# Performance work log

Hardware: AMD Instinct MI355X
Metric: run time of the kernel (lower is better)

## Reference

```python
import jax, jax.numpy as jnp
import numpy as np

N_NODES = 50000
N_EDGES = 800000
IN_FEATS = 128
HIDDEN = 256
N_CLASSES = 64


def setup_inputs() -> dict:
    key = jax.random.key(0)
    ks = jax.random.split(key, 16)
    def w(k, shape, fan_in):
        return jax.random.normal(k, shape, dtype=jnp.float32) * (1.0 / np.sqrt(fan_in))
    inp = {
        "x": jax.random.normal(ks[0], (N_NODES, IN_FEATS), dtype=jnp.float32),
        "edge_src": jax.random.randint(ks[1], (N_EDGES,), 0, N_NODES, dtype=jnp.int32),
        "edge_dst": jax.random.randint(ks[2], (N_EDGES,), 0, N_NODES, dtype=jnp.int32),
        # layer 0: in_feats -> hidden
        "W0s": w(ks[3], (IN_FEATS, HIDDEN), IN_FEATS),
        "W0n": w(ks[4], (IN_FEATS, HIDDEN), IN_FEATS),
        "b0": jnp.zeros((HIDDEN,), dtype=jnp.float32),
        # layer 1: hidden -> hidden
        "W1s": w(ks[5], (HIDDEN, HIDDEN), HIDDEN),
        "W1n": w(ks[6], (HIDDEN, HIDDEN), HIDDEN),
        "b1": jnp.zeros((HIDDEN,), dtype=jnp.float32),
        # layer 2: hidden -> hidden (last conv also outputs hidden per source code)
        "W2s": w(ks[7], (HIDDEN, HIDDEN), HIDDEN),
        "W2n": w(ks[8], (HIDDEN, HIDDEN), HIDDEN),
        "b2": jnp.zeros((HIDDEN,), dtype=jnp.float32),
        # fc1: hidden -> n_classes
        "Wfc": w(ks[9], (HIDDEN, N_CLASSES), HIDDEN),
        "bfc": jnp.zeros((N_CLASSES,), dtype=jnp.float32),
    }
    return inp


def _sage_layer(h, src, dst, Ws, Wn, b):
    # mean-neighbor aggregation: segment-sum messages, divide by in-degree
    msg = h[src]  # [E, D] irregular gather
    agg = jax.ops.segment_sum(msg, dst, num_segments=N_NODES)  # [N, D]
    deg = jax.ops.segment_sum(jnp.ones_like(dst, dtype=h.dtype), dst, num_segments=N_NODES)
    h_neigh = agg / jnp.maximum(deg, 1.0)[:, None]
    # DGL SAGEConv (mean): fc_self(h) + fc_neigh(h_neigh) + bias
    return h @ Ws + h_neigh @ Wn + b


def reference(x, edge_src, edge_dst, W0s, W0n, b0, W1s, W1n, b1, W2s, W2n, b2, Wfc, bfc):
    # forward applies dropout (identity at eval) and NO activation between layers,
    # matching the original module's forward().
    h = _sage_layer(x, edge_src, edge_dst, W0s, W0n, b0)
    h = _sage_layer(h, edge_src, edge_dst, W1s, W1n, b1)
    h = _sage_layer(h, edge_src, edge_dst, W2s, W2n, b2)
    return h @ Wfc + bfc  # [N, n_classes]
```

## Files before the change

kernel.cpp:

```cpp
#include <hip/hip_runtime.h>

#define NN 50000
#define NE 800000
#define F_IN 128
#define HID 256
#define N_CLS 64
#define SCAN_BLOCKS ((NN + 255) / 256)
#define HEPT 2
#define HBF ((NE + 256 * HEPT - 1) / (256 * HEPT))
#define CF_BLOCKS 36
#define CL_BLOCKS 9
#define GA_BLOCKS ((NN + 127) / 128)
#define GG_BLOCKS ((NN + 31) / 32)
#define CROWS 515

typedef _Float16 half8 __attribute__((ext_vector_type(8)));
typedef float f32x4 __attribute__((ext_vector_type(4)));

__device__ __forceinline__ const float* virtC1_row(int r, const float* W0s,
                                                   const float* W0n, const float* b0) {
    if (r < 0) return nullptr;
    if (r < 128) return W0s + (size_t)r * 256;
    if (r < 256) return W0n + (size_t)(r - 128) * 256;
    if (r == 512) return b0;
    return nullptr;
}

__device__ __forceinline__ int shift_src(int r) {
    if (r >= 128 && r < 512) return r - 128;
    if (r == 513) return 512;
    if (r == 514) return 513;
    return -1;
}

__device__ __forceinline__ void compose_first_dev(
    int bx, const float* __restrict__ W0s, const float* __restrict__ W0n,
    const float* __restrict__ b0,
    const float* __restrict__ B1, const float* __restrict__ B2,
    const float* __restrict__ brow, float* __restrict__ C)
{
    __shared__ float As[64][17];
    __shared__ float Bs[16][64];
    const int tid = threadIdx.x;
    const int tx = tid & 15, ty = tid >> 4;
    const int row0 = (bx % 9) * 64;
    const int col0 = (bx / 9) * 64;
    const int lr = tid >> 2, lc = tid & 3;
    const int br = tid >> 4, bc = tid & 15;

    const int grow = row0 + lr;
    const int srcr0 = (grow < CROWS) ? grow : -1;
    const float* ap0 = virtC1_row(srcr0, W0s, W0n, b0);
    const float* ap1 = virtC1_row(shift_src(grow), W0s, W0n, b0);

    float acc[4][4] = {};

    float4 av = ap0 ? *(const float4*)(ap0 + lc * 4) : make_float4(0.f, 0.f, 0.f, 0.f);
    float4 bv = *(const float4*)(B1 + (size_t)br * 256 + col0 + bc * 4);

    for (int s = 0; s < 32; ++s) {
        As[lr][lc * 4 + 0] = av.x;
        As[lr][lc * 4 + 1] = av.y;
        As[lr][lc * 4 + 2] = av.z;
        As[lr][lc * 4 + 3] = av.w;
        *(float4*)&Bs[br][bc * 4] = bv;
        __syncthreads();
        if (s + 1 < 32) {
            int pass = (s + 1) >> 4;
            int k0 = ((s + 1) & 15) << 4;
            const float* ap = pass ? ap1 : ap0;
            const float* B = pass ? B2 : B1;
            av = ap ? *(const float4*)(ap + k0 + lc * 4) : make_float4(0.f, 0.f, 0.f, 0.f);
            bv = *(const float4*)(B + (size_t)(k0 + br) * 256 + col0 + bc * 4);
        }
        #pragma unroll
        for (int k = 0; k < 16; ++k) {
            float a[4];
            #pragma unroll
            for (int i = 0; i < 4; ++i) a[i] = As[ty * 4 + i][k];
            float4 bb = *(const float4*)&Bs[k][tx * 4];
            const float b[4] = {bb.x, bb.y, bb.z, bb.w};
            #pragma unroll
            for (int i = 0; i < 4; ++i)
                #pragma unroll
                for (int j = 0; j < 4; ++j)
                    acc[i][j] += a[i] * b[j];
        }
        __syncthreads();
    }

    #pragma unroll
    for (int i = 0; i < 4; ++i) {
        int r = row0 + ty * 4 + i;
        if (r < CROWS) {
            #pragma unroll
            for (int j = 0; j < 4; ++j) {
                float v = acc[i][j];
                if (r == 512) v += brow[col0 + tx * 4 + j];
                C[(size_t)r * 256 + col0 + tx * 4 + j] = v;
            }
        }
    }
}

__device__ __forceinline__ void compose_mid_dev(
    int bx, const float* __restrict__ A,
    const float* __restrict__ B1, const float* __restrict__ B2,
    const float* __restrict__ brow, float* __restrict__ C)
{
    __shared__ float As[64][17];
    __shared__ float Bs[16][64];
    const int tid = threadIdx.x;
    const int tx = tid & 15, ty = tid >> 4;
    const int row0 = (bx % 9) * 64;
    const int col0 = (bx / 9) * 64;
    const int lr = tid >> 2, lc = tid & 3;
    const int br = tid >> 4, bc = tid & 15;

    const int grow = row0 + lr;
    const int p0 = (grow < CROWS) ? grow : -1;
    const int p1 = shift_src(grow);

    float acc[4][4] = {};

    float4 av = (p0 >= 0) ? *(const float4*)(A + (size_t)p0 * 256 + lc * 4)
                          : make_float4(0.f, 0.f, 0.f, 0.f);
    float4 bv = *(const float4*)(B1 + (size_t)br * 256 + col0 + bc * 4);

    for (int s = 0; s < 32; ++s) {
        As[lr][lc * 4 + 0] = av.x;
        As[lr][lc * 4 + 1] = av.y;
        As[lr][lc * 4 + 2] = av.z;
        As[lr][lc * 4 + 3] = av.w;
        *(float4*)&Bs[br][bc * 4] = bv;
        __syncthreads();
        if (s + 1 < 32) {
            int pass = (s + 1) >> 4;
            int k0 = ((s + 1) & 15) << 4;
            int p = pass ? p1 : p0;
            const float* B = pass ? B2 : B1;
            av = (p >= 0) ? *(const float4*)(A + (size_t)p * 256 + k0 + lc * 4)
                          : make_float4(0.f, 0.f, 0.f, 0.f);
            bv = *(const float4*)(B + (size_t)(k0 + br) * 256 + col0 + bc * 4);
        }
        #pragma unroll
        for (int k = 0; k < 16; ++k) {
            float a[4];
            #pragma unroll
            for (int i = 0; i < 4; ++i) a[i] = As[ty * 4 + i][k];
            float4 bb = *(const float4*)&Bs[k][tx * 4];
            const float b[4] = {bb.x, bb.y, bb.z, bb.w};
            #pragma unroll
            for (int i = 0; i < 4; ++i)
                #pragma unroll
                for (int j = 0; j < 4; ++j)
                    acc[i][j] += a[i] * b[j];
        }
        __syncthreads();
    }

    #pragma unroll
    for (int i = 0; i < 4; ++i) {
        int r = row0 + ty * 4 + i;
        if (r < CROWS) {
            #pragma unroll
            for (int j = 0; j < 4; ++j) {
                float v = acc[i][j];
                if (r == 512) v += brow[col0 + tx * 4 + j];
                C[(size_t)r * 256 + col0 + tx * 4 + j] = v;
            }
        }
    }
}

__device__ __forceinline__ void compose_last_dev(
    int bx, const float* __restrict__ A, const float* __restrict__ B1,
    const float* __restrict__ brow, float* __restrict__ Vf, _Float16* __restrict__ BT)
{
    __shared__ float As[64][17];
    __shared__ float Bs[16][64];
    const int tid = threadIdx.x;
    const int tx = tid & 15, ty = tid >> 4;
    const int row0 = bx * 64;
    const int lr = tid >> 2, lc = tid & 3;
    const int br = tid >> 4, bc = tid & 15;

    const int grow = row0 + lr;
    const float* ap = (grow < CROWS) ? (A + (size_t)grow * 256) : nullptr;

    float acc[4][4] = {};

    float4 av = ap ? *(const float4*)(ap + lc * 4) : make_float4(0.f, 0.f, 0.f, 0.f);
    float4 bv = *(const float4*)(B1 + (size_t)br * 64 + bc * 4);

    for (int s = 0; s < 16; ++s) {
        As[lr][lc * 4 + 0] = av.x;
        As[lr][lc * 4 + 1] = av.y;
        As[lr][lc * 4 + 2] = av.z;
        As[lr][lc * 4 + 3] = av.w;
        *(float4*)&Bs[br][bc * 4] = bv;
        __syncthreads();
        if (s + 1 < 16) {
            int k0 = (s + 1) << 4;
            av = ap ? *(const float4*)(ap + k0 + lc * 4) : make_float4(0.f, 0.f, 0.f, 0.f);
            bv = *(const float4*)(B1 + (size_t)(k0 + br) * 64 + bc * 4);
        }
        #pragma unroll
        for (int k = 0; k < 16; ++k) {
            float a[4];
            #pragma unroll
            for (int i = 0; i < 4; ++i) a[i] = As[ty * 4 + i][k];
            float4 bb = *(const float4*)&Bs[k][tx * 4];
            const float b[4] = {bb.x, bb.y, bb.z, bb.w};
            #pragma unroll
            for (int i = 0; i < 4; ++i)
                #pragma unroll
                for (int j = 0; j < 4; ++j)
                    acc[i][j] += a[i] * b[j];
        }
        __syncthreads();
    }

    #pragma unroll
    for (int i = 0; i < 4; ++i) {
        int r = row0 + ty * 4 + i;
        if (r < CROWS) {
            #pragma unroll
            for (int j = 0; j < 4; ++j) {
                int c = tx * 4 + j;
                float v = acc[i][j];
                if (r == 512) v += brow[c];
                Vf[(size_t)r * 64 + c] = v;
                if (r < 512)
                    BT[(size_t)((r >> 7) * 64 + c) * 128 + (r & 127)] = (_Float16)v;
            }
        }
    }
}

__device__ __forceinline__ void hist_dev(int bx, const int* __restrict__ edst,
                                         int* __restrict__ cnt,
                                         unsigned short* __restrict__ rank) {
    int base = bx * (256 * HEPT) + threadIdx.x;
    int d[HEPT];
    #pragma unroll
    for (int k = 0; k < HEPT; ++k) {
        int e = base + k * 256;
        d[k] = (e < NE) ? edst[e] : -1;
    }
    #pragma unroll
    for (int k = 0; k < HEPT; ++k) {
        int e = base + k * 256;
        if (d[k] >= 0) rank[e] = (unsigned short)atomicAdd(&cnt[d[k]], 1);
    }
}

__device__ __forceinline__ void scan_block_sums_dev(const int* __restrict__ cnt,
                                                    int* __restrict__ blockSums, int n, int bx) {
    __shared__ int s[256];
    int t = threadIdx.x;
    int i = bx * 256 + t;
    s[t] = (i < n) ? cnt[i] : 0;
    __syncthreads();
    for (int off = 128; off > 0; off >>= 1) {
        if (t < off) s[t] += s[t + off];
        __syncthreads();
    }
    if (t == 0) blockSums[bx] = s[0];
}

__device__ __forceinline__ void scan_final2_dev(const int* __restrict__ cnt,
                                                const int* __restrict__ blockSums,
                                                int* __restrict__ offs,
                                                float* __restrict__ dinv, int n, int bx) {
    __shared__ int s[256];
    __shared__ int base_sh;
    int t = threadIdx.x;
    s[t] = (t < SCAN_BLOCKS) ? blockSums[t] : 0;
    __syncthreads();
    for (int off = 1; off < 256; off <<= 1) {
        int v = (t >= off) ? s[t - off] : 0;
        __syncthreads();
        s[t] += v;
        __syncthreads();
    }
    if (t == 0) base_sh = (bx > 0) ? s[bx - 1] : 0;
    __syncthreads();
    int base = base_sh;
    __syncthreads();
    int i = bx * 256 + t;
    int v = (i < n) ? cnt[i] : 0;
    s[t] = v;
    __syncthreads();
    for (int off = 1; off < 256; off <<= 1) {
        int u = (t >= off) ? s[t - off] : 0;
        __syncthreads();
        s[t] += u;
        __syncthreads();
    }
    if (i < n) {
        offs[i] = base + s[t] - v;
        dinv[i] = 1.0f / (float)max(v, 1);
    }
    if (i == n - 1) offs[n] = base + s[t];
}

__device__ __forceinline__ void gemm_y_dev(
    int bx, int by,
    const float* __restrict__ X, const _Float16* __restrict__ BT,
    _Float16* __restrict__ Y, _Float16* __restrict__ Tc, int N)
{
    constexpr int LP = 40;
    __shared__ _Float16 As[128 * LP];
    __shared__ _Float16 Bs[128 * LP];

    const int tid = threadIdx.x;
    const int wave = tid >> 6;
    const int lane = tid & 63;
    const int l15 = lane & 15;
    const int quad = lane >> 4;
    const int wrow = wave >> 1;
    const int wcol = wave & 1;
    const int m_base = wrow * 64;
    const int n_base = wcol * 64;

    const int row0 = bx * 128;
    const int col0 = by * 128;

    f32x4 acc[4][4] = {};

    for (int k0 = 0; k0 < 128; k0 += 32) {
        #pragma unroll
        for (int r = 0; r < 2; ++r) {
            int idx = r * 256 + tid;
            int row = idx >> 2, ch = idx & 3;
            int gr = row0 + row; if (gr > N - 1) gr = N - 1;
            const float* ap = X + (size_t)gr * 128 + k0 + ch * 8;
            float4 f0 = *(const float4*)ap;
            float4 f1 = *(const float4*)(ap + 4);
            half8 v = { (_Float16)f0.x, (_Float16)f0.y, (_Float16)f0.z, (_Float16)f0.w,
                        (_Float16)f1.x, (_Float16)f1.y, (_Float16)f1.z, (_Float16)f1.w };
            *(half8*)&As[row * LP + ch * 8] = v;
        }
        #pragma unroll
        for (int r = 0; r < 2; ++r) {
            int idx = r * 256 + tid;
            int row = idx >> 2, ch = idx & 3;
            *(half8*)&Bs[row * LP + ch * 8] =
                *(const half8*)(BT + (size_t)(col0 + row) * 128 + k0 + ch * 8);
        }
        __syncthreads();
        half8 af[4], bf[4];
        #pragma unroll
        for (int i = 0; i < 4; ++i)
            af[i] = *(const half8*)&As[(m_base + i * 16 + l15) * LP + quad * 8];
        #pragma unroll
        for (int j = 0; j < 4; ++j)
            bf[j] = *(const half8*)&Bs[(n_base + j * 16 + l15) * LP + quad * 8];
        #pragma unroll
        for (int i = 0; i < 4; ++i)
            #pragma unroll
            for (int j = 0; j < 4; ++j)
                acc[i][j] = __builtin_amdgcn_mfma_f32_16x16x32_f16(af[i], bf[j], acc[i][j], 0, 0, 0);
        __syncthreads();
    }

    #pragma unroll
    for (int i = 0; i < 4; ++i) {
        #pragma unroll
        for (int j = 0; j < 4; ++j) {
            int col = col0 + n_base + j * 16 + l15;
            #pragma unroll
            for (int r = 0; r < 4; ++r) {
                int row = row0 + m_base + i * 16 + quad * 4 + r;
                if (row < N) {
                    _Float16 v = (_Float16)acc[i][j][r];
                    Y[(size_t)row * 256 + col] = v;
                    if (col >= 192) Tc[(size_t)row * 64 + (col - 192)] = v;
                }
            }
        }
    }
}

template <bool OUT_F32>
__device__ __forceinline__ void gather_node_dev(
    int node, int lane,
    const _Float16* __restrict__ Tin,
    const unsigned short* __restrict__ csr, const int* __restrict__ offs,
    const float* __restrict__ dinv,
    const _Float16* __restrict__ Yadd,
    const float* __restrict__ cvec,
    void* __restrict__ Tout)
{
    int beg = offs[node], end = offs[node + 1];
    float acc[8] = {};
    int e = beg;
    for (; e + 7 < end; e += 8) {
        int s0 = csr[e], s1 = csr[e + 1], s2 = csr[e + 2], s3 = csr[e + 3];
        int s4 = csr[e + 4], s5 = csr[e + 5], s6 = csr[e + 6], s7 = csr[e + 7];
        half8 v0 = *(const half8*)(Tin + (size_t)s0 * 64 + lane * 8);
        half8 v1 = *(const half8*)(Tin + (size_t)s1 * 64 + lane * 8);
        half8 v2 = *(const half8*)(Tin + (size_t)s2 * 64 + lane * 8);
        half8 v3 = *(const half8*)(Tin + (size_t)s3 * 64 + lane * 8);
        half8 v4 = *(const half8*)(Tin + (size_t)s4 * 64 + lane * 8);
        half8 v5 = *(const half8*)(Tin + (size_t)s5 * 64 + lane * 8);
        half8 v6 = *(const half8*)(Tin + (size_t)s6 * 64 + lane * 8);
        half8 v7 = *(const half8*)(Tin + (size_t)s7 * 64 + lane * 8);
        #pragma unroll
        for (int j = 0; j < 8; ++j)
            acc[j] += (((float)v0[j] + (float)v1[j]) + ((float)v2[j] + (float)v3[j]))
                    + (((float)v4[j] + (float)v5[j]) + ((float)v6[j] + (float)v7[j]));
    }
    for (; e + 3 < end; e += 4) {
        int s0 = csr[e], s1 = csr[e + 1], s2 = csr[e + 2], s3 = csr[e + 3];
        half8 v0 = *(const half8*)(Tin + (size_t)s0 * 64 + lane * 8);
        half8 v1 = *(const half8*)(Tin + (size_t)s1 * 64 + lane * 8);
        half8 v2 = *(const half8*)(Tin + (size_t)s2 * 64 + lane * 8);
        half8 v3 = *(const half8*)(Tin + (size_t)s3 * 64 + lane * 8);
        #pragma unroll
        for (int j = 0; j < 8; ++j)
            acc[j] += ((float)v0[j] + (float)v1[j]) + ((float)v2[j] + (float)v3[j]);
    }
    for (; e < end; ++e) {
        half8 v = *(const half8*)(Tin + (size_t)csr[e] * 64 + lane * 8);
        #pragma unroll
        for (int j = 0; j < 8; ++j) acc[j] += (float)v[j];
    }
    float sc = dinv[node];
    half8 y = *(const half8*)(Yadd + (size_t)node * 256 + lane * 8);
    if (OUT_F32) {
        float* o = (float*)Tout + (size_t)node * 64 + lane * 8;
        float4 o0, o1;
        o0.x = acc[0] * sc + (float)y[0] + cvec[lane * 8 + 0];
        o0.y = acc[1] * sc + (float)y[1] + cvec[lane * 8 + 1];
        o0.z = acc[2] * sc + (float)y[2] + cvec[lane * 8 + 2];
        o0.w = acc[3] * sc + (float)y[3] + cvec[lane * 8 + 3];
        o1.x = acc[4] * sc + (float)y[4] + cvec[lane * 8 + 4];
        o1.y = acc[5] * sc + (float)y[5] + cvec[lane * 8 + 5];
        o1.z = acc[6] * sc + (float)y[6] + cvec[lane * 8 + 6];
        o1.w = acc[7] * sc + (float)y[7] + cvec[lane * 8 + 7];
        *(float4*)o = o0;
        *(float4*)(o + 4) = o1;
    } else {
        half8 o;
        #pragma unroll
        for (int j = 0; j < 8; ++j)
            o[j] = (_Float16)(acc[j] * sc + (float)y[j] + cvec[lane * 8 + j]);
        *(half8*)((_Float16*)Tout + (size_t)node * 64 + lane * 8) = o;
    }
}

__global__ __launch_bounds__(256) void k_composeF_hist(
    const int* __restrict__ edst, int* __restrict__ cnt, unsigned short* __restrict__ rank,
    const float* __restrict__ W0s, const float* __restrict__ W0n, const float* __restrict__ b0,
    const float* __restrict__ W1s, const float* __restrict__ W1n, const float* __restrict__ b1,
    float* __restrict__ C2)
{
    if (blockIdx.x < CF_BLOCKS) {
        compose_first_dev(blockIdx.x, W0s, W0n, b0, W1s, W1n, b1, C2);
    } else {
        hist_dev(blockIdx.x - CF_BLOCKS, edst, cnt, rank);
    }
}

__global__ __launch_bounds__(256) void k_composeM_scanA(
    const int* __restrict__ cnt, int* __restrict__ blockSums,
    const float* __restrict__ C2,
    const float* __restrict__ W2s, const float* __restrict__ W2n, const float* __restrict__ b2,
    float* __restrict__ C3)
{
    if (blockIdx.x < CF_BLOCKS) compose_mid_dev(blockIdx.x, C2, W2s, W2n, b2, C3);
    else scan_block_sums_dev(cnt, blockSums, NN, blockIdx.x - CF_BLOCKS);
}

__global__ __launch_bounds__(256) void k_composeL_scanF(
    const int* __restrict__ cnt, const int* __restrict__ blockSums,
    int* __restrict__ offs, float* __restrict__ dinv,
    const float* __restrict__ C3, const float* __restrict__ Wfc, const float* __restrict__ bfc,
    float* __restrict__ Vf, _Float16* __restrict__ BT)
{
    if (blockIdx.x < CL_BLOCKS) compose_last_dev(blockIdx.x, C3, Wfc, bfc, Vf, BT);
    else scan_final2_dev(cnt, blockSums, offs, dinv, NN, blockIdx.x - CL_BLOCKS);
}

__global__ __launch_bounds__(256) void k_gemmT_place(
    const int* __restrict__ esrc, const int* __restrict__ edst,
    const unsigned short* __restrict__ rank, const int* __restrict__ offs,
    unsigned short* __restrict__ csr,
    const float* __restrict__ X, const _Float16* __restrict__ BT,
    _Float16* __restrict__ Y, _Float16* __restrict__ Tc)
{
    if (blockIdx.x < GA_BLOCKS) {
        gemm_y_dev(blockIdx.x, 1, X, BT, Y, Tc, NN);
    } else {
        int base = (blockIdx.x - GA_BLOCKS) * (256 * HEPT) + threadIdx.x;
        int d[HEPT], s[HEPT], r[HEPT];
        #pragma unroll
        for (int k = 0; k < HEPT; ++k) {
            int e = base + k * 256;
            if (e < NE) { d[k] = edst[e]; s[k] = esrc[e]; r[k] = rank[e]; }
            else d[k] = -1;
        }
        #pragma unroll
        for (int k = 0; k < HEPT; ++k) {
            if (d[k] >= 0) csr[offs[d[k]] + r[k]] = (unsigned short)s[k];
        }
    }
}

__global__ __launch_bounds__(256) void k_gemmA_gather1(
    const float* __restrict__ X, const _Float16* __restrict__ BT,
    _Float16* __restrict__ Y, _Float16* __restrict__ Tc,
    const unsigned short* __restrict__ csr, const int* __restrict__ offs,
    const float* __restrict__ dinv, const float* __restrict__ Vf,
    _Float16* __restrict__ Ta)
{
    if (blockIdx.x < GA_BLOCKS) {
        gemm_y_dev(blockIdx.x, 0, X, BT, Y, Tc, NN);
    } else {
        int node = (blockIdx.x - GA_BLOCKS) * 32 + (threadIdx.x >> 3);
        int lane = threadIdx.x & 7;
        if (node < NN)
            gather_node_dev<false>(node, lane, Tc, csr, offs, dinv,
                                   Y + 128, Vf + (size_t)514 * 64, (void*)Ta);
    }
}

template <bool OUT_F32>
__global__ __launch_bounds__(256) void gather64(
    const _Float16* __restrict__ Tin,
    const unsigned short* __restrict__ csr, const int* __restrict__ offs,
    const float* __restrict__ dinv,
    const _Float16* __restrict__ Yadd,
    const float* __restrict__ cvec,
    void* __restrict__ Tout, int N)
{
    int node = blockIdx.x * 32 + (threadIdx.x >> 3);
    int lane = threadIdx.x & 7;
    if (node >= N) return;
    gather_node_dev<OUT_F32>(node, lane, Tin, csr, offs, dinv, Yadd, cvec, Tout);
}

extern "C" void kernel_launch(void* const* d_in, const int* in_sizes, int n_in,
                              void* d_out, int out_size, void* d_ws, size_t ws_size,
                              hipStream_t stream) {
    const float* x    = (const float*)d_in[0];
    const int*   esrc = (const int*)d_in[1];
    const int*   edst = (const int*)d_in[2];
    const float* W0s  = (const float*)d_in[3];
    const float* W0n  = (const float*)d_in[4];
    const float* b0   = (const float*)d_in[5];
    const float* W1s  = (const float*)d_in[6];
    const float* W1n  = (const float*)d_in[7];
    const float* b1   = (const float*)d_in[8];
    const float* W2s  = (const float*)d_in[9];
    const float* W2n  = (const float*)d_in[10];
    const float* b2   = (const float*)d_in[11];
    const float* Wfc  = (const float*)d_in[12];
    const float* bfc  = (const float*)d_in[13];
    float* out = (float*)d_out;

    _Float16* Y   = (_Float16*)d_ws;
    _Float16* Ta  = Y + (size_t)NN * 256;
    _Float16* Tb  = Ta + (size_t)NN * 64;
    _Float16* Tc  = Tb + (size_t)NN * 64;
    _Float16* BT  = Tc + (size_t)NN * 64;
    float* C2     = (float*)(BT + 256 * 128);
    float* C3     = C2 + CROWS * 256;
    float* Vf     = C3 + CROWS * 256;
    float* dinv   = Vf + CROWS * 64;
    int* cnt      = (int*)(dinv + NN);
    int* offs     = cnt + NN;
    int* blockSums = offs + NN + 1;
    unsigned short* rank = (unsigned short*)(blockSums + SCAN_BLOCKS);
    unsigned short* csr  = rank + NE;

    hipMemsetAsync(cnt, 0, (size_t)NN * sizeof(int), stream);

    k_composeF_hist<<<CF_BLOCKS + HBF, 256, 0, stream>>>(
        edst, cnt, rank, W0s, W0n, b0, W1s, W1n, b1, C2);

    k_composeM_scanA<<<CF_BLOCKS + SCAN_BLOCKS, 256, 0, stream>>>(
        cnt, blockSums, C2, W2s, W2n, b2, C3);

    k_composeL_scanF<<<CL_BLOCKS + SCAN_BLOCKS, 256, 0, stream>>>(
        cnt, blockSums, offs, dinv, C3, Wfc, bfc, Vf, BT);

    k_gemmT_place<<<GA_BLOCKS + HBF, 256, 0, stream>>>(
        esrc, edst, rank, offs, csr, x, BT, Y, Tc);

    k_gemmA_gather1<<<GA_BLOCKS + GG_BLOCKS, 256, 0, stream>>>(
        x, BT, Y, Tc, csr, offs, dinv, Vf, Ta);

    gather64<false><<<GG_BLOCKS, 256, 0, stream>>>(
        Ta, csr, offs, dinv, Y + 64, Vf + (size_t)513 * 64, (void*)Tb, NN);
    gather64<true><<<GG_BLOCKS, 256, 0, stream>>>(
        Tb, csr, offs, dinv, Y, Vf + (size_t)512 * 64, (void*)out, NN);
}
```

Measured before the change: 272.2 us.

## Split edge histogram across two compose kernels and fuse scan into one pass

The degree histogram is split into two halves, the first running alongside the first weight-composition kernel and the second alongside the middle one, so each compose stage overlaps with atomic histogram work. The two-pass block-sum scan is replaced by a single-pass scan in which each block redundantly sums every count before its own range to get its base offset. This removes one scan stage and balances work across the compose kernels. The cost is redundant reads of the count array that grow with block index, up to about 50K ints for the last block.

```diff
diff --git a/kernel.cpp b/kernel.cpp
--- a/kernel.cpp
+++ b/kernel.cpp
@@ -2,12 +2,14 @@
 
 #define NN 50000
 #define NE 800000
+#define NE_HALF 400000
 #define F_IN 128
 #define HID 256
 #define N_CLS 64
 #define SCAN_BLOCKS ((NN + 255) / 256)
 #define HEPT 2
 #define HBF ((NE + 256 * HEPT - 1) / (256 * HEPT))
+#define HBH ((NE_HALF + 256 * HEPT - 1) / (256 * HEPT))
 #define CF_BLOCKS 36
 #define CL_BLOCKS 9
 #define GA_BLOCKS ((NN + 127) / 128)
@@ -238,15 +240,17 @@
     }
 }
 
-__device__ __forceinline__ void hist_dev(int bx, const int* __restrict__ edst,
+__device__ __forceinline__ void hist_dev(int bx, int start, int count,
+                                         const int* __restrict__ edst,
                                          int* __restrict__ cnt,
                                          unsigned short* __restrict__ rank) {
-    int base = bx * (256 * HEPT) + threadIdx.x;
+    int base = start + bx * (256 * HEPT) + threadIdx.x;
+    int lim = start + count;
     int d[HEPT];
     #pragma unroll
     for (int k = 0; k < HEPT; ++k) {
         int e = base + k * 256;
-        d[k] = (e < NE) ? edst[e] : -1;
+        d[k] = (e < lim) ? edst[e] : -1;
     }
     #pragma unroll
     for (int k = 0; k < HEPT; ++k) {
@@ -255,41 +259,24 @@
     }
 }
 
-__device__ __forceinline__ void scan_block_sums_dev(const int* __restrict__ cnt,
-                                                    int* __restrict__ blockSums, int n, int bx) {
+__device__ __forceinline__ void scan_full_dev(const int* __restrict__ cnt,
+                                              int* __restrict__ offs,
+                                              float* __restrict__ dinv, int bx) {
     __shared__ int s[256];
-    int t = threadIdx.x;
-    int i = bx * 256 + t;
-    s[t] = (i < n) ? cnt[i] : 0;
+    const int t = threadIdx.x;
+    const int limit = bx * 256;
+    int p = 0;
+    for (int i = t; i < limit; i += 256) p += cnt[i];
+    s[t] = p;
     __syncthreads();
     for (int off = 128; off > 0; off >>= 1) {
         if (t < off) s[t] += s[t + off];
         __syncthreads();
     }
-    if (t == 0) blockSums[bx] = s[0];
-}
-
-__device__ __forceinline__ void scan_final2_dev(const int* __restrict__ cnt,
-                                                const int* __restrict__ blockSums,
-                                                int* __restrict__ offs,
-                                                float* __restrict__ dinv, int n, int bx) {
-    __shared__ int s[256];
-    __shared__ int base_sh;
-    int t = threadIdx.x;
-    s[t] = (t < SCAN_BLOCKS) ? blockSums[t] : 0;
+    const int base = s[0];
     __syncthreads();
-    for (int off = 1; off < 256; off <<= 1) {
-        int v = (t >= off) ? s[t - off] : 0;
-        __syncthreads();
-        s[t] += v;
-        __syncthreads();
-    }
-    if (t == 0) base_sh = (bx > 0) ? s[bx - 1] : 0;
-    __syncthreads();
-    int base = base_sh;
-    __syncthreads();
-    int i = bx * 256 + t;
-    int v = (i < n) ? cnt[i] : 0;
+    int i = limit + t;
+    int v = (i < NN) ? cnt[i] : 0;
     s[t] = v;
     __syncthreads();
     for (int off = 1; off < 256; off <<= 1) {
@@ -298,11 +285,11 @@
         s[t] += u;
         __syncthreads();
     }
-    if (i < n) {
+    if (i < NN) {
         offs[i] = base + s[t] - v;
         dinv[i] = 1.0f / (float)max(v, 1);
     }
-    if (i == n - 1) offs[n] = base + s[t];
+    if (i == NN - 1) offs[NN] = base + s[t];
 }
 
 __device__ __forceinline__ void gemm_y_dev(
@@ -460,28 +447,27 @@
     if (blockIdx.x < CF_BLOCKS) {
         compose_first_dev(blockIdx.x, W0s, W0n, b0, W1s, W1n, b1, C2);
     } else {
-        hist_dev(blockIdx.x - CF_BLOCKS, edst, cnt, rank);
-    }
-}
-
-__global__ __launch_bounds__(256) void k_composeM_scanA(
-    const int* __restrict__ cnt, int* __restrict__ blockSums,
+        hist_dev(blockIdx.x - CF_BLOCKS, 0, NE_HALF, edst, cnt, rank);
+    }
+}
+
+__global__ __launch_bounds__(256) void k_composeM_hist2(
+    const int* __restrict__ edst, int* __restrict__ cnt, unsigned short* __restrict__ rank,
     const float* __restrict__ C2,
     const float* __restrict__ W2s, const float* __restrict__ W2n, const float* __restrict__ b2,
     float* __restrict__ C3)
 {
     if (blockIdx.x < CF_BLOCKS) compose_mid_dev(blockIdx.x, C2, W2s, W2n, b2, C3);
-    else scan_block_sums_dev(cnt, blockSums, NN, blockIdx.x - CF_BLOCKS);
-}
-
-__global__ __launch_bounds__(256) void k_composeL_scanF(
-    const int* __restrict__ cnt, const int* __restrict__ blockSums,
-    int* __restrict__ offs, float* __restrict__ dinv,
+    else hist_dev(blockIdx.x - CF_BLOCKS, NE_HALF, NE - NE_HALF, edst, cnt, rank);
+}
+
+__global__ __launch_bounds__(256) void k_composeL_scan(
+    const int* __restrict__ cnt, int* __restrict__ offs, float* __restrict__ dinv,
     const float* __restrict__ C3, const float* __restrict__ Wfc, const float* __restrict__ bfc,
     float* __restrict__ Vf, _Float16* __restrict__ BT)
 {
     if (blockIdx.x < CL_BLOCKS) compose_last_dev(blockIdx.x, C3, Wfc, bfc, Vf, BT);
-    else scan_final2_dev(cnt, blockSums, offs, dinv, NN, blockIdx.x - CL_BLOCKS);
+    else scan_full_dev(cnt, offs, dinv, blockIdx.x - CL_BLOCKS);
 }
 
 __global__ __launch_bounds__(256) void k_gemmT_place(
@@ -578,14 +564,14 @@
 
     hipMemsetAsync(cnt, 0, (size_t)NN * sizeof(int), stream);
 
-    k_composeF_hist<<<CF_BLOCKS + HBF, 256, 0, stream>>>(
+    k_composeF_hist<<<CF_BLOCKS + HBH, 256, 0, stream>>>(
         edst, cnt, rank, W0s, W0n, b0, W1s, W1n, b1, C2);
 
-    k_composeM_scanA<<<CF_BLOCKS + SCAN_BLOCKS, 256, 0, stream>>>(
-        cnt, blockSums, C2, W2s, W2n, b2, C3);
-
-    k_composeL_scanF<<<CL_BLOCKS + SCAN_BLOCKS, 256, 0, stream>>>(
-        cnt, blockSums, offs, dinv, C3, Wfc, bfc, Vf, BT);
+    k_composeM_hist2<<<CF_BLOCKS + HBH, 256, 0, stream>>>(
+        edst, cnt, rank, C2, W2s, W2n, b2, C3);
+
+    k_composeL_scan<<<CL_BLOCKS + SCAN_BLOCKS, 256, 0, stream>>>(
+        cnt, offs, dinv, C3, Wfc, bfc, Vf, BT);
 
     k_gemmT_place<<<GA_BLOCKS + HBF, 256, 0, stream>>>(
         esrc, edst, rank, offs, csr, x, BT, Y, Tc);
```

After: 284.4 us. 1.04x slower.
